# Optimization experiments

Hardware: AMD Instinct MI355X
Metric: run time of the kernel (lower is better)

The kernel has to match this reference:

```python
import jax, jax.numpy as jnp
import numpy as np

EMBED_DIM = 512
NUM_HEADS = 8
HEAD_DIM = EMBED_DIM // NUM_HEADS


def setup_inputs() -> dict:
    key = jax.random.key(0)
    ks = jax.random.split(key, 9)
    s = 1.0 / np.sqrt(EMBED_DIM)
    x = jax.random.normal(ks[0], (2, 4096, EMBED_DIM), dtype=jnp.float32)
    return {
        "x": x,
        "Wq": jax.random.uniform(ks[1], (EMBED_DIM, EMBED_DIM), jnp.float32, -s, s),
        "bq": jax.random.uniform(ks[2], (EMBED_DIM,), jnp.float32, -s, s),
        "Wk": jax.random.uniform(ks[3], (EMBED_DIM, EMBED_DIM), jnp.float32, -s, s),
        "bk": jax.random.uniform(ks[4], (EMBED_DIM,), jnp.float32, -s, s),
        "Wv": jax.random.uniform(ks[5], (EMBED_DIM, EMBED_DIM), jnp.float32, -s, s),
        "bv": jax.random.uniform(ks[6], (EMBED_DIM,), jnp.float32, -s, s),
        "Wo": jax.random.uniform(ks[7], (EMBED_DIM, EMBED_DIM), jnp.float32, -s, s),
        "bo": jax.random.uniform(ks[8], (EMBED_DIM,), jnp.float32, -s, s),
    }


def reference(x, Wq, bq, Wk, bk, Wv, bv, Wo, bo):
    B, S, E = x.shape
    H, D = NUM_HEADS, HEAD_DIM
    # projections (torch Linear: x @ W.T + b)
    q = (x @ Wq.T + bq).reshape(B, S, H, D).transpose(0, 2, 1, 3)  # [B,H,S,D]
    k = (x @ Wk.T + bk).reshape(B, S, H, D).transpose(0, 2, 1, 3)
    v = (x @ Wv.T + bv).reshape(B, S, H, D).transpose(0, 2, 1, 3)
    scores = jnp.einsum("bhsd,bhtd->bhst", q, k) / np.sqrt(D)  # [B,H,S,S]
    attn = jax.nn.softmax(scores, axis=-1)
    out = jnp.einsum("bhst,bhtd->bhsd", attn, v)  # [B,H,S,D]
    out = out.transpose(0, 2, 1, 3).reshape(B, S, E)
    return out @ Wo.T + bo + x
```

## Files before the change

kernel.cpp:

```cpp
#include <hip/hip_runtime.h>
#include <hip/hip_bf16.h>


typedef __attribute__((ext_vector_type(8))) short short8;
typedef __attribute__((ext_vector_type(4))) short short4v;
typedef __attribute__((ext_vector_type(4))) float floatx4;
typedef __attribute__((ext_vector_type(2))) float floatx2;

#define SEQ 4096
#define EMB 512
#define NH 8
#define HD 64
#define MROWS 8192
#define SC2 0.18033688011112042f

__device__ inline unsigned short f2bf_rne(float f) {
    union { float f; unsigned int u; } c; c.f = f;
    unsigned int u = c.u;
    return (unsigned short)((u + 0x7FFFu + ((u >> 16) & 1u)) >> 16);
}

__device__ inline short8 load8f(const float* __restrict__ p) {
    float4 a = *(const float4*)p;
    float4 b = *(const float4*)(p + 4);
    short8 r;
    r[0] = (short)f2bf_rne(a.x); r[1] = (short)f2bf_rne(a.y);
    r[2] = (short)f2bf_rne(a.z); r[3] = (short)f2bf_rne(a.w);
    r[4] = (short)f2bf_rne(b.x); r[5] = (short)f2bf_rne(b.y);
    r[6] = (short)f2bf_rne(b.z); r[7] = (short)f2bf_rne(b.w);
    return r;
}

__device__ inline void gload_lds16(const unsigned short* g, unsigned short* l) {
    __builtin_amdgcn_global_load_lds(
        (__attribute__((address_space(1))) void*)(void*)g,
        (__attribute__((address_space(3))) void*)l,
        16, 0, 0);
}

__device__ inline unsigned int pk_bf2(float a, float b) {
    union { float f; unsigned int u; } ca, cb; ca.f = a; cb.f = b;
    return __builtin_amdgcn_perm(cb.u + 0x8000u, ca.u + 0x8000u, 0x07060302u);
}

__device__ inline unsigned int pk_bf2t(float a, float b) {
    union { float f; unsigned int u; } ca, cb; ca.f = a; cb.f = b;
    return __builtin_amdgcn_perm(cb.u, ca.u, 0x07060302u);
}

__global__ __launch_bounds__(256) void convert_kernel(
    const float* __restrict__ x, const float* __restrict__ Wq,
    const float* __restrict__ Wk, const float* __restrict__ Wv,
    const float* __restrict__ Wo, unsigned short* __restrict__ xb,
    unsigned short* __restrict__ wb)
{
    const size_t i8 = ((size_t)blockIdx.x * 256 + threadIdx.x) * 8;
    const float* src; unsigned short* dst;
    if (i8 < (size_t)MROWS * EMB) { src = x + i8; dst = xb + i8; }
    else {
        size_t j = i8 - (size_t)MROWS * EMB;
        int w = (int)(j >> 18); size_t off = j & 262143;
        src = (w == 0 ? Wq : w == 1 ? Wk : w == 2 ? Wv : Wo) + off;
        dst = wb + (size_t)w * 262144 + off;
    }
    *(short8*)dst = load8f(src);
}

__global__ __launch_bounds__(256) void qkv_kernel(
    const unsigned short* __restrict__ xb, const unsigned short* __restrict__ wb,
    const float* __restrict__ bq, const float* __restrict__ bk,
    const float* __restrict__ bv, unsigned short* __restrict__ Qo,
    unsigned short* __restrict__ Ko, unsigned short* __restrict__ VTo)
{
    __shared__ unsigned short smem[32768];

    const int tid = threadIdx.x, wave = tid >> 6, lane = tid & 63;
    const int quad = lane >> 4, l16 = lane & 15;
    const int wm = wave >> 1, wn = wave & 1;
    const int row0 = blockIdx.x * 128, col0 = blockIdx.y * 128;
    const int z = blockIdx.z;

    unsigned short* sA = smem;
    unsigned short* sB = smem + 16384;

    const unsigned short* A = xb + (size_t)row0 * EMB;
    const unsigned short* Bm = wb + (size_t)z * 262144 + (size_t)col0 * EMB;
    const float* bias = z == 0 ? bq : z == 1 ? bk : bv;
    unsigned short* out = z == 0 ? Qo : z == 1 ? Ko : VTo;

    auto stage = [&](int buf, int k0) {
#pragma unroll
        for (int it = 0; it < 4; ++it) {
            const int s = it * 256 + tid;
            const int row = s >> 3, cg = (s & 7) ^ (row & 7);
            const size_t go = (size_t)row * EMB + k0 + cg * 8;
            gload_lds16(A + go, &sA[buf * 8192 + (it * 256 + wave * 64) * 8]);
            gload_lds16(Bm + go, &sB[buf * 8192 + (it * 256 + wave * 64) * 8]);
        }
    };

    floatx4 acc[4][4];
#pragma unroll
    for (int i = 0; i < 4; ++i)
#pragma unroll
        for (int j = 0; j < 4; ++j) { floatx4 zz = {0.f,0.f,0.f,0.f}; acc[i][j] = zz; }

    stage(0, 0);
    int buf = 0;
    for (int k0 = 0; k0 < EMB; k0 += 64) {
        __syncthreads();
        if (k0 + 64 < EMB) stage(buf ^ 1, k0 + 64);
#pragma unroll
        for (int kk = 0; kk < 2; ++kk) {
            short8 a[4], b[4];
#pragma unroll
            for (int mi = 0; mi < 4; ++mi)
                a[mi] = *(const short8*)&sA[buf * 8192 + (wm * 64 + mi * 16 + l16) * 64 + (((kk * 4 + quad) ^ (l16 & 7)) << 3)];
#pragma unroll
            for (int ni = 0; ni < 4; ++ni)
                b[ni] = *(const short8*)&sB[buf * 8192 + (wn * 64 + ni * 16 + l16) * 64 + (((kk * 4 + quad) ^ (l16 & 7)) << 3)];
            if (z != 2) {
#pragma unroll
                for (int i = 0; i < 4; ++i)
#pragma unroll
                    for (int j = 0; j < 4; ++j)
                        acc[i][j] = __builtin_amdgcn_mfma_f32_16x16x32_bf16(b[i], a[j], acc[i][j], 0, 0, 0);
            } else {
#pragma unroll
                for (int i = 0; i < 4; ++i)
#pragma unroll
                    for (int j = 0; j < 4; ++j)
                        acc[i][j] = __builtin_amdgcn_mfma_f32_16x16x32_bf16(a[i], b[j], acc[i][j], 0, 0, 0);
            }
        }
        buf ^= 1;
    }

    __syncthreads();
    unsigned short* ct = smem;
    const float qs = (z == 0) ? SC2 : 1.0f;
    if (z != 2) {
#pragma unroll
        for (int i = 0; i < 4; ++i) {
            const int n0 = wn * 64 + i * 16 + quad * 4;
            const float4 fb = *(const float4*)&bias[col0 + n0];
#pragma unroll
            for (int j = 0; j < 4; ++j) {
                const int m = wm * 64 + j * 16 + l16;
                ushort4 pk;
                pk.x = f2bf_rne((acc[i][j][0] + fb.x) * qs);
                pk.y = f2bf_rne((acc[i][j][1] + fb.y) * qs);
                pk.z = f2bf_rne((acc[i][j][2] + fb.z) * qs);
                pk.w = f2bf_rne((acc[i][j][3] + fb.w) * qs);
                *(ushort4*)&ct[m * 132 + n0] = pk;
            }
        }
    } else {
#pragma unroll
        for (int j = 0; j < 4; ++j) {
            const int n = wn * 64 + j * 16 + l16;
            const float fb = bias[col0 + n];
#pragma unroll
            for (int i = 0; i < 4; ++i) {
                const int m0 = wm * 64 + i * 16 + quad * 4;
                ushort4 pk;
                pk.x = f2bf_rne(acc[i][j][0] + fb);
                pk.y = f2bf_rne(acc[i][j][1] + fb);
                pk.z = f2bf_rne(acc[i][j][2] + fb);
                pk.w = f2bf_rne(acc[i][j][3] + fb);
                *(ushort4*)&ct[n * 132 + m0] = pk;
            }
        }
    }
    __syncthreads();
#pragma unroll
    for (int it = 0; it < 8; ++it) {
        const int idx = it * 256 + tid;
        const int row = idx >> 4, chunk = idx & 15;
        short8 v = *(const short8*)&ct[row * 132 + chunk * 8];
        size_t addr;
        if (z != 2) {
            const int m_g = row0 + row;
            const int b = m_g >> 12, s = m_g & 4095;
            const int n_g = col0 + chunk * 8;
            const int h = n_g >> 6, d = n_g & 63;
            addr = ((size_t)((b * NH + h) * SEQ + s)) * HD + d;
        } else {
            const int n_g = col0 + row;
            const int h = n_g >> 6, d = n_g & 63;
            const int m_g = row0 + chunk * 8;
            const int b = m_g >> 12, s0 = m_g & 4095;
            addr = ((size_t)((b * NH + h) * HD + d)) * SEQ + s0;
        }
        *(short8*)&out[addr] = v;
    }
}

__global__ __launch_bounds__(256) void attn_kernel(
    const unsigned short* __restrict__ Q, const unsigned short* __restrict__ K,
    const unsigned short* __restrict__ VT, unsigned short* __restrict__ Oout)
{
    __shared__ unsigned short sK[2][2][4096];
    __shared__ unsigned short sVT[2][2][4096];

    const int tid = threadIdx.x, wave = tid >> 6, lane = tid & 63;
    const int quad = lane >> 4, l16 = lane & 15;
    const int bh = blockIdx.x, q0 = blockIdx.y * 128;
    const int xm = l16 & 7;

    const unsigned short* Qh = Q + (size_t)bh * SEQ * HD;
    const unsigned short* Kh = K + (size_t)bh * SEQ * HD;
    const unsigned short* Vh = VT + (size_t)bh * HD * SEQ;

    short8 qf[2][2];
#pragma unroll
    for (int mi = 0; mi < 2; ++mi)
#pragma unroll
        for (int kk = 0; kk < 2; ++kk)
            qf[mi][kk] = *(const short8*)(Qh + (size_t)(q0 + wave * 32 + mi * 16 + l16) * HD + kk * 32 + quad * 8);

    int kbase[4], kx0[4], kx1[4];
#pragma unroll
    for (int nt = 0; nt < 4; ++nt) {
        const int g = nt >> 1, T = nt & 1;
        const int R = g * 32 + ((l16 >> 2) << 3) + (T << 2) + (l16 & 3);
        const int fR = (R & 7) ^ ((R >> 2) & 7);
        kbase[nt] = R * 64;
        kx0[nt] = (quad ^ fR) << 3;
        kx1[nt] = ((4 + quad) ^ fR) << 3;
    }

    floatx4 oacc[2][4];
#pragma unroll
    for (int mi = 0; mi < 2; ++mi)
#pragma unroll
        for (int dt = 0; dt < 4; ++dt) { floatx4 zz = {0.f,0.f,0.f,0.f}; oacc[mi][dt] = zz; }
    floatx2 psum2[2] = {{0.f, 0.f}, {0.f, 0.f}};
    const floatx4 z4 = {0.f, 0.f, 0.f, 0.f};

    auto stage = [&](int buf, int t0) {
#pragma unroll
        for (int sub = 0; sub < 2; ++sub)
#pragma unroll
            for (int psi = 0; psi < 2; ++psi) {
                const int r = psi * 32 + wave * 8 + (lane >> 3);
                const int j = lane & 7;
                const int cK = j ^ ((r & 7) ^ ((r >> 2) & 7));
                const int cV = j ^ (r & 7);
                gload_lds16(Kh + (size_t)(t0 + sub * 64 + r) * HD + cK * 8,
                            &sK[buf][sub][psi * 2048 + wave * 512]);
                gload_lds16(Vh + (size_t)r * SEQ + t0 + sub * 64 + cV * 8,
                            &sVT[buf][sub][psi * 2048 + wave * 512]);
            }
    };

    stage(0, 0);
    int buf = 0;
    for (int t0 = 0; t0 < SEQ; t0 += 128) {
        __syncthreads();
        if (t0 + 128 < SEQ) stage(buf ^ 1, t0 + 128);

#pragma unroll
        for (int sub = 0; sub < 2; ++sub) {
            const unsigned short* sKs  = sK[buf][sub];
            const unsigned short* sVTs = sVT[buf][sub];

            floatx4 stf[2][4];
            {
                short8 bK[4];
#pragma unroll
                for (int nt = 0; nt < 4; ++nt)
                    bK[nt] = *(const short8*)&sKs[kbase[nt] + kx0[nt]];
#pragma unroll
                for (int mi = 0; mi < 2; ++mi)
#pragma unroll
                    for (int nt = 0; nt < 4; ++nt)
                        stf[mi][nt] = __builtin_amdgcn_mfma_f32_16x16x32_bf16(bK[nt], qf[mi][0], z4, 0, 0, 0);
            }
            {
                short8 bK[4];
#pragma unroll
                for (int nt = 0; nt < 4; ++nt)
                    bK[nt] = *(const short8*)&sKs[kbase[nt] + kx1[nt]];
#pragma unroll
                for (int mi = 0; mi < 2; ++mi)
#pragma unroll
                    for (int nt = 0; nt < 4; ++nt)
                        stf[mi][nt] = __builtin_amdgcn_mfma_f32_16x16x32_bf16(bK[nt], qf[mi][1], stf[mi][nt], 0, 0, 0);
            }

            short8 bvAll[2][4];
#pragma unroll
            for (int g = 0; g < 2; ++g)
#pragma unroll
                for (int dt = 0; dt < 4; ++dt)
                    bvAll[g][dt] = *(const short8*)&sVTs[(dt * 16 + l16) * 64 + (((g * 4 + quad) ^ xm) << 3)];

            short8 paf[2][2];
#pragma unroll
            for (int mi = 0; mi < 2; ++mi)
#pragma unroll
                for (int g = 0; g < 2; ++g) {
                    float e[8];
#pragma unroll
                    for (int T = 0; T < 2; ++T)
#pragma unroll
                        for (int r = 0; r < 4; ++r)
                            e[T * 4 + r] = __builtin_amdgcn_exp2f(stf[mi][g * 2 + T][r]);
                    floatx2 pa = {e[0], e[1]}, pb = {e[2], e[3]};
                    floatx2 pc = {e[4], e[5]}, pd = {e[6], e[7]};
                    psum2[mi] += (pa + pb) + (pc + pd);
                    union { uint4 u; short8 s; } cv;
                    cv.u.x = pk_bf2t(e[0], e[1]);
                    cv.u.y = pk_bf2t(e[2], e[3]);
                    cv.u.z = pk_bf2t(e[4], e[5]);
                    cv.u.w = pk_bf2t(e[6], e[7]);
                    paf[mi][g] = cv.s;
                }

#pragma unroll
            for (int g = 0; g < 2; ++g)
#pragma unroll
                for (int mi = 0; mi < 2; ++mi)
#pragma unroll
                    for (int dt = 0; dt < 4; ++dt)
                        oacc[mi][dt] = __builtin_amdgcn_mfma_f32_16x16x32_bf16(paf[mi][g], bvAll[g][dt], oacc[mi][dt], 0, 0, 0);
        }
        buf ^= 1;
    }

    float psum[2];
#pragma unroll
    for (int mi = 0; mi < 2; ++mi) {
        psum[mi] = psum2[mi][0] + psum2[mi][1];
        psum[mi] += __shfl_xor(psum[mi], 16);
        psum[mi] += __shfl_xor(psum[mi], 32);
    }

    const int b = bh >> 3, h = bh & 7;
#pragma unroll
    for (int mi = 0; mi < 2; ++mi)
#pragma unroll
        for (int r = 0; r < 4; ++r) {
            const float inv = 1.0f / __shfl(psum[mi], quad * 4 + r);
            const int s = q0 + wave * 32 + mi * 16 + quad * 4 + r;
            const size_t base = ((size_t)b * SEQ + s) * EMB + h * HD;
#pragma unroll
            for (int dt = 0; dt < 4; ++dt)
                Oout[base + dt * 16 + l16] = f2bf_rne(oacc[mi][dt][r] * inv);
        }
}

__global__ __launch_bounds__(256) void outproj_kernel(
    const unsigned short* __restrict__ Ain, const unsigned short* __restrict__ wob,
    const float* __restrict__ bias, const float* __restrict__ X,
    float* __restrict__ out)
{
    __shared__ unsigned short sA[2][4096];
    __shared__ unsigned short sB[2][8192];

    const int tid = threadIdx.x, wave = tid >> 6, lane = tid & 63;
    const int quad = lane >> 4, l16 = lane & 15;
    const int wm = wave >> 1, wn = wave & 1;
    const int row0 = blockIdx.x * 64, col0 = blockIdx.y * 128;

    const unsigned short* A = Ain + (size_t)row0 * EMB;
    const unsigned short* Bm = wob + (size_t)col0 * EMB;

    auto stage = [&](int buf, int k0) {
#pragma unroll
        for (int it = 0; it < 2; ++it) {
            const int s = it * 256 + tid;
            const int row = s >> 3, cg = (s & 7) ^ (row & 7);
            gload_lds16(A + (size_t)row * EMB + k0 + cg * 8, &sA[buf][(it * 256 + wave * 64) * 8]);
        }
#pragma unroll
        for (int it = 0; it < 4; ++it) {
            const int s = it * 256 + tid;
            const int row = s >> 3, cg = (s & 7) ^ (row & 7);
            gload_lds16(Bm + (size_t)row * EMB + k0 + cg * 8, &sB[buf][(it * 256 + wave * 64) * 8]);
        }
    };

    floatx4 acc[2][4];
#pragma unroll
    for (int mi = 0; mi < 2; ++mi)
#pragma unroll
        for (int ni = 0; ni < 4; ++ni) { floatx4 zz = {0.f,0.f,0.f,0.f}; acc[mi][ni] = zz; }

    stage(0, 0);
    int buf = 0;
    for (int k0 = 0; k0 < EMB; k0 += 64) {
        __syncthreads();
        if (k0 + 64 < EMB) stage(buf ^ 1, k0 + 64);
#pragma unroll
        for (int kk = 0; kk < 2; ++kk) {
            short8 a[2], b[4];
#pragma unroll
            for (int mi = 0; mi < 2; ++mi)
                a[mi] = *(const short8*)&sA[buf][(wm * 32 + mi * 16 + l16) * 64 + (((kk * 4 + quad) ^ (l16 & 7)) << 3)];
#pragma unroll
            for (int ni = 0; ni < 4; ++ni)
                b[ni] = *(const short8*)&sB[buf][(wn * 64 + ni * 16 + l16) * 64 + (((kk * 4 + quad) ^ (l16 & 7)) << 3)];
#pragma unroll
            for (int mi = 0; mi < 2; ++mi)
#pragma unroll
                for (int ni = 0; ni < 4; ++ni)
                    acc[mi][ni] = __builtin_amdgcn_mfma_f32_16x16x32_bf16(a[mi], b[ni], acc[mi][ni], 0, 0, 0);
        }
        buf ^= 1;
    }

#pragma unroll
    for (int mi = 0; mi < 2; ++mi)
#pragma unroll
        for (int ni = 0; ni < 4; ++ni) {
            const int n = col0 + wn * 64 + ni * 16 + l16;
            const float bs = bias[n];
#pragma unroll
            for (int r = 0; r < 4; ++r) {
                const int m = row0 + wm * 32 + mi * 16 + quad * 4 + r;
                const size_t idx = (size_t)m * EMB + n;
                out[idx] = acc[mi][ni][r] + bs + X[idx];
            }
        }
}

extern "C" void kernel_launch(void* const* d_in, const int* in_sizes, int n_in,
                              void* d_out, int out_size, void* d_ws, size_t ws_size,
                              hipStream_t stream) {
    const float* x  = (const float*)d_in[0];
    const float* Wq = (const float*)d_in[1];
    const float* bq = (const float*)d_in[2];
    const float* Wk = (const float*)d_in[3];
    const float* bk = (const float*)d_in[4];
    const float* Wv = (const float*)d_in[5];
    const float* bv = (const float*)d_in[6];
    const float* Wo = (const float*)d_in[7];
    const float* bo = (const float*)d_in[8];
    float* out = (float*)d_out;

    const size_t SZ = (size_t)MROWS * EMB;
    unsigned short* wsXB = (unsigned short*)d_ws;
    unsigned short* wsWB = wsXB + SZ;
    unsigned short* wsQ  = wsWB + 4 * 262144;
    unsigned short* wsK  = wsQ + SZ;
    unsigned short* wsVT = wsK + SZ;

    convert_kernel<<<2560, 256, 0, stream>>>(x, Wq, Wk, Wv, Wo, wsXB, wsWB);
    qkv_kernel<<<dim3(MROWS / 128, EMB / 128, 3), 256, 0, stream>>>(
        wsXB, wsWB, bq, bk, bv, wsQ, wsK, wsVT);
    attn_kernel<<<dim3(2 * NH, SEQ / 128), 256, 0, stream>>>(wsQ, wsK, wsVT, wsXB);
    outproj_kernel<<<dim3(MROWS / 64, EMB / 128), 256, 0, stream>>>(
        wsXB, wsWB + 3 * 262144, bo, x, out);
}
```

Measured before the change: 193.9 us.

## Halve attention KV tile, raise occupancy, compute row sums via MFMA with ones

```diff
diff --git a/kernel.cpp b/kernel.cpp
--- a/kernel.cpp
+++ b/kernel.cpp
@@ -196,12 +196,12 @@
     }
 }
 
-__global__ __launch_bounds__(256) void attn_kernel(
+__global__ __launch_bounds__(256, 4) void attn_kernel(
     const unsigned short* __restrict__ Q, const unsigned short* __restrict__ K,
     const unsigned short* __restrict__ VT, unsigned short* __restrict__ Oout)
 {
-    __shared__ unsigned short sK[2][2][4096];
-    __shared__ unsigned short sVT[2][2][4096];
+    __shared__ unsigned short sK[2][4096];
+    __shared__ unsigned short sVT[2][4096];
 
     const int tid = threadIdx.x, wave = tid >> 6, lane = tid & 63;
     const int quad = lane >> 4, l16 = lane & 15;
@@ -235,114 +235,104 @@
     for (int mi = 0; mi < 2; ++mi)
 #pragma unroll
         for (int dt = 0; dt < 4; ++dt) { floatx4 zz = {0.f,0.f,0.f,0.f}; oacc[mi][dt] = zz; }
-    floatx2 psum2[2] = {{0.f, 0.f}, {0.f, 0.f}};
+    floatx4 sacc[2];
+#pragma unroll
+    for (int mi = 0; mi < 2; ++mi) { floatx4 zz = {0.f,0.f,0.f,0.f}; sacc[mi] = zz; }
     const floatx4 z4 = {0.f, 0.f, 0.f, 0.f};
+    const short ob = (short)0x3F80;
+    const short8 ones8 = {ob, ob, ob, ob, ob, ob, ob, ob};
 
     auto stage = [&](int buf, int t0) {
 #pragma unroll
-        for (int sub = 0; sub < 2; ++sub)
-#pragma unroll
-            for (int psi = 0; psi < 2; ++psi) {
-                const int r = psi * 32 + wave * 8 + (lane >> 3);
-                const int j = lane & 7;
-                const int cK = j ^ ((r & 7) ^ ((r >> 2) & 7));
-                const int cV = j ^ (r & 7);
-                gload_lds16(Kh + (size_t)(t0 + sub * 64 + r) * HD + cK * 8,
-                            &sK[buf][sub][psi * 2048 + wave * 512]);
-                gload_lds16(Vh + (size_t)r * SEQ + t0 + sub * 64 + cV * 8,
-                            &sVT[buf][sub][psi * 2048 + wave * 512]);
-            }
+        for (int psi = 0; psi < 2; ++psi) {
+            const int r = psi * 32 + wave * 8 + (lane >> 3);
+            const int j = lane & 7;
+            const int cK = j ^ ((r & 7) ^ ((r >> 2) & 7));
+            const int cV = j ^ (r & 7);
+            gload_lds16(Kh + (size_t)(t0 + r) * HD + cK * 8,
+                        &sK[buf][psi * 2048 + wave * 512]);
+            gload_lds16(Vh + (size_t)r * SEQ + t0 + cV * 8,
+                        &sVT[buf][psi * 2048 + wave * 512]);
+        }
     };
 
     stage(0, 0);
     int buf = 0;
-    for (int t0 = 0; t0 < SEQ; t0 += 128) {
+    for (int t0 = 0; t0 < SEQ; t0 += 64) {
         __syncthreads();
-        if (t0 + 128 < SEQ) stage(buf ^ 1, t0 + 128);
-
-#pragma unroll
-        for (int sub = 0; sub < 2; ++sub) {
-            const unsigned short* sKs  = sK[buf][sub];
-            const unsigned short* sVTs = sVT[buf][sub];
-
-            floatx4 stf[2][4];
-            {
-                short8 bK[4];
+        if (t0 + 64 < SEQ) stage(buf ^ 1, t0 + 64);
+
+        const unsigned short* sKs  = sK[buf];
+        const unsigned short* sVTs = sVT[buf];
+
+        floatx4 stf[2][4];
+        {
+            short8 bK[4];
+#pragma unroll
+            for (int nt = 0; nt < 4; ++nt)
+                bK[nt] = *(const short8*)&sKs[kbase[nt] + kx0[nt]];
+#pragma unroll
+            for (int mi = 0; mi < 2; ++mi)
 #pragma unroll
                 for (int nt = 0; nt < 4; ++nt)
-                    bK[nt] = *(const short8*)&sKs[kbase[nt] + kx0[nt]];
-#pragma unroll
-                for (int mi = 0; mi < 2; ++mi)
-#pragma unroll
-                    for (int nt = 0; nt < 4; ++nt)
-                        stf[mi][nt] = __builtin_amdgcn_mfma_f32_16x16x32_bf16(bK[nt], qf[mi][0], z4, 0, 0, 0);
-            }
-            {
-                short8 bK[4];
+                    stf[mi][nt] = __builtin_amdgcn_mfma_f32_16x16x32_bf16(bK[nt], qf[mi][0], z4, 0, 0, 0);
+        }
+        {
+            short8 bK[4];
+#pragma unroll
+            for (int nt = 0; nt < 4; ++nt)
+                bK[nt] = *(const short8*)&sKs[kbase[nt] + kx1[nt]];
+#pragma unroll
+            for (int mi = 0; mi < 2; ++mi)
 #pragma unroll
                 for (int nt = 0; nt < 4; ++nt)
-                    bK[nt] = *(const short8*)&sKs[kbase[nt] + kx1[nt]];
-#pragma unroll
-                for (int mi = 0; mi < 2; ++mi)
-#pragma unroll
-                    for (int nt = 0; nt < 4; ++nt)
-                        stf[mi][nt] = __builtin_amdgcn_mfma_f32_16x16x32_bf16(bK[nt], qf[mi][1], stf[mi][nt], 0, 0, 0);
-            }
-
-            short8 bvAll[2][4];
-#pragma unroll
-            for (int g = 0; g < 2; ++g)
+                    stf[mi][nt] = __builtin_amdgcn_mfma_f32_16x16x32_bf16(bK[nt], qf[mi][1], stf[mi][nt], 0, 0, 0);
+        }
+
+        short8 bvAll[2][4];
+#pragma unroll
+        for (int g = 0; g < 2; ++g)
+#pragma unroll
+            for (int dt = 0; dt < 4; ++dt)
+                bvAll[g][dt] = *(const short8*)&sVTs[(dt * 16 + l16) * 64 + (((g * 4 + quad) ^ xm) << 3)];
+
+        short8 paf[2][2];
+#pragma unroll
+        for (int mi = 0; mi < 2; ++mi)
+#pragma unroll
+            for (int g = 0; g < 2; ++g) {
+                float e[8];
+#pragma unroll
+                for (int T = 0; T < 2; ++T)
+#pragma unroll
+                    for (int r = 0; r < 4; ++r)
+                        e[T * 4 + r] = __builtin_amdgcn_exp2f(stf[mi][g * 2 + T][r]);
+                union { uint4 u; short8 s; } cv;
+                cv.u.x = pk_bf2t(e[0], e[1]);
+                cv.u.y = pk_bf2t(e[2], e[3]);
+                cv.u.z = pk_bf2t(e[4], e[5]);
+                cv.u.w = pk_bf2t(e[6], e[7]);
+                paf[mi][g] = cv.s;
+            }
+
+#pragma unroll
+        for (int g = 0; g < 2; ++g)
+#pragma unroll
+            for (int mi = 0; mi < 2; ++mi) {
+                sacc[mi] = __builtin_amdgcn_mfma_f32_16x16x32_bf16(paf[mi][g], ones8, sacc[mi], 0, 0, 0);
 #pragma unroll
                 for (int dt = 0; dt < 4; ++dt)
-                    bvAll[g][dt] = *(const short8*)&sVTs[(dt * 16 + l16) * 64 + (((g * 4 + quad) ^ xm) << 3)];
-
-            short8 paf[2][2];
-#pragma unroll
-            for (int mi = 0; mi < 2; ++mi)
-#pragma unroll
-                for (int g = 0; g < 2; ++g) {
-                    float e[8];
-#pragma unroll
-                    for (int T = 0; T < 2; ++T)
-#pragma unroll
-                        for (int r = 0; r < 4; ++r)
-                            e[T * 4 + r] = __builtin_amdgcn_exp2f(stf[mi][g * 2 + T][r]);
-                    floatx2 pa = {e[0], e[1]}, pb = {e[2], e[3]};
-                    floatx2 pc = {e[4], e[5]}, pd = {e[6], e[7]};
-                    psum2[mi] += (pa + pb) + (pc + pd);
-                    union { uint4 u; short8 s; } cv;
-                    cv.u.x = pk_bf2t(e[0], e[1]);
-                    cv.u.y = pk_bf2t(e[2], e[3]);
-                    cv.u.z = pk_bf2t(e[4], e[5]);
-                    cv.u.w = pk_bf2t(e[6], e[7]);
-                    paf[mi][g] = cv.s;
-                }
-
-#pragma unroll
-            for (int g = 0; g < 2; ++g)
-#pragma unroll
-                for (int mi = 0; mi < 2; ++mi)
-#pragma unroll
-                    for (int dt = 0; dt < 4; ++dt)
-                        oacc[mi][dt] = __builtin_amdgcn_mfma_f32_16x16x32_bf16(paf[mi][g], bvAll[g][dt], oacc[mi][dt], 0, 0, 0);
-        }
+                    oacc[mi][dt] = __builtin_amdgcn_mfma_f32_16x16x32_bf16(paf[mi][g], bvAll[g][dt], oacc[mi][dt], 0, 0, 0);
+            }
         buf ^= 1;
     }
 
-    float psum[2];
-#pragma unroll
-    for (int mi = 0; mi < 2; ++mi) {
-        psum[mi] = psum2[mi][0] + psum2[mi][1];
-        psum[mi] += __shfl_xor(psum[mi], 16);
-        psum[mi] += __shfl_xor(psum[mi], 32);
-    }
-
     const int b = bh >> 3, h = bh & 7;
 #pragma unroll
     for (int mi = 0; mi < 2; ++mi)
 #pragma unroll
         for (int r = 0; r < 4; ++r) {
-            const float inv = 1.0f / __shfl(psum[mi], quad * 4 + r);
+            const float inv = 1.0f / sacc[mi][r];
             const int s = q0 + wave * 32 + mi * 16 + quad * 4 + r;
             const size_t base = ((size_t)b * SEQ + s) * EMB + h * HD;
 #pragma unroll
```

After: 185.3 us. 1.05x faster.
